# Performance work log

Hardware: AMD Instinct MI355X
Metric: run time of the kernel (lower is better)

## Reference

```python
import jax, jax.numpy as jnp
import numpy as np


def setup_inputs() -> dict:
    key = jax.random.key(0)
    ip = jax.random.normal(key, (8, 256, 128, 128), dtype=jnp.float32)
    return {"ip": ip}


def reference(ip):
    b, C, H, W = ip.shape
    two_c = 2 * C
    # precomputed complex shift grid: exp(-1j*2*pi*(C-0.5)*v/(2C)), v = 0..2C-1
    v = jnp.arange(two_c, dtype=jnp.float32)
    angle = -2.0 * jnp.pi * (C - 0.5) * v / two_c
    shift = (jnp.cos(angle) + 1j * jnp.sin(angle)).astype(jnp.complex64)  # [2C]

    viDct = ip * two_c                                   # [b, C, H, W]
    flip_neg = -viDct[:, 1:][:, ::-1]                    # [b, C-1, H, W]
    zeros = jnp.zeros((b, 1, H, W), dtype=ip.dtype)
    rev = jnp.concatenate([viDct, zeros, flip_neg], axis=1)  # [b, 2C, H, W]
    rev = rev.astype(jnp.complex64) * shift[None, :, None, None]
    vxx = jnp.fft.ifft(rev, axis=1)                      # norm='backward' (default)
    out = vxx[:, :C][:, ::-1].real                       # first C, flipped, real part
    return out.astype(ip.dtype)
```

## Files before the change

kernel.cpp:

```cpp
#include <hip/hip_runtime.h>
#include <hip/hip_bf16.h>
#include <math.h>

#define NB   8
#define NC   256
#define NHW  (128 * 128)

#define BM 128
#define BN 128
#define BK 32
#define LSTR 80

typedef __attribute__((ext_vector_type(4))) float f32x4;
typedef __attribute__((ext_vector_type(8))) short bf16x8;

__device__ __forceinline__ unsigned short f2bf(float f) {
    unsigned u = __builtin_bit_cast(unsigned, f);
    u += 0x7fffu + ((u >> 16) & 1u);
    return (unsigned short)(u >> 16);
}

__global__ void coef_kernel(unsigned short* __restrict__ coef) {
    int idx = blockIdx.x * 256 + threadIdx.x;
    int c = idx >> 8;
    int k = idx & 255;
    int t = (k * (2 * c + 1)) & 1023;
    float v = (k == 0) ? 1.0f : 2.0f * cosf((float)t * (float)(M_PI / 512.0));
    coef[idx] = f2bf(v);
}

__global__ __launch_bounds__(256, 2)
void dct_gemm(const float* __restrict__ X, const unsigned short* __restrict__ Mcoef,
              float* __restrict__ Out) {
    __shared__ unsigned char lds[2 * BM * LSTR];
    unsigned char* Alds = lds;
    unsigned char* Xlds = lds + BM * LSTR;

    const int tid  = threadIdx.x;
    const int lane = tid & 63;
    const int wave = tid >> 6;
    const int wm   = wave >> 1;
    const int wn   = wave & 1;
    const int m16  = lane & 15;
    const int quad = lane >> 4;

    const int p0 = blockIdx.x * BN;
    const int c0 = blockIdx.y * BM;
    const int bbase = blockIdx.z * (NC * NHW);

    const float* Xb = X + bbase;
    float* Ob = Out + bbase;

    const int sr = tid & 127;
    const int sh = tid >> 7;

    f32x4 acc[4][4];
#pragma unroll
    for (int i = 0; i < 4; i++)
#pragma unroll
        for (int j = 0; j < 4; j++) acc[i][j] = (f32x4){0.f, 0.f, 0.f, 0.f};

    for (int k0 = 0; k0 < NC; k0 += BK) {
        __syncthreads();

        {
            const unsigned short* src = Mcoef + (c0 + sr) * NC + k0 + sh * 16;
            int4 a0 = *(const int4*)(src);
            int4 a1 = *(const int4*)(src + 8);
            unsigned char* dst = Alds + sr * LSTR + sh * 32;
            *(int4*)(dst)      = a0;
            *(int4*)(dst + 16) = a1;
        }

        {
            const float* src = Xb + (k0 + sh * 16) * NHW + p0 + sr;
            float v[16];
#pragma unroll
            for (int j = 0; j < 16; j++) v[j] = src[j * NHW];
            unsigned pk[8];
#pragma unroll
            for (int j = 0; j < 8; j++) {
                unsigned lo = __builtin_bit_cast(unsigned, v[2 * j]);
                lo += 0x7fffu + ((lo >> 16) & 1u);
                unsigned hi = __builtin_bit_cast(unsigned, v[2 * j + 1]);
                hi += 0x7fffu + ((hi >> 16) & 1u);
                pk[j] = (lo >> 16) | (hi & 0xffff0000u);
            }
            unsigned char* dst = Xlds + sr * LSTR + sh * 32;
            *(int4*)(dst)      = (int4){(int)pk[0], (int)pk[1], (int)pk[2], (int)pk[3]};
            *(int4*)(dst + 16) = (int4){(int)pk[4], (int)pk[5], (int)pk[6], (int)pk[7]};
        }

        __syncthreads();

        bf16x8 afrag[4], bfrag[4];
#pragma unroll
        for (int mt = 0; mt < 4; mt++) {
            int row = wm * 64 + mt * 16 + m16;
            afrag[mt] = *(const bf16x8*)(Alds + row * LSTR + quad * 16);
        }
#pragma unroll
        for (int nt = 0; nt < 4; nt++) {
            int row = wn * 64 + nt * 16 + m16;
            bfrag[nt] = *(const bf16x8*)(Xlds + row * LSTR + quad * 16);
        }
#pragma unroll
        for (int mt = 0; mt < 4; mt++)
#pragma unroll
            for (int nt = 0; nt < 4; nt++)
                acc[mt][nt] = __builtin_amdgcn_mfma_f32_16x16x32_bf16(
                    afrag[mt], bfrag[nt], acc[mt][nt], 0, 0, 0);
    }

#pragma unroll
    for (int mt = 0; mt < 4; mt++) {
#pragma unroll
        for (int nt = 0; nt < 4; nt++) {
            int cc = c0 + wm * 64 + mt * 16 + quad * 4;
            int pp = p0 + wn * 64 + nt * 16 + m16;
            float* o = Ob + cc * NHW + pp;
#pragma unroll
            for (int r = 0; r < 4; r++)
                o[r * NHW] = acc[mt][nt][r];
        }
    }
}

extern "C" void kernel_launch(void* const* d_in, const int* in_sizes, int n_in,
                              void* d_out, int out_size, void* d_ws, size_t ws_size,
                              hipStream_t stream) {
    const float* ip = (const float*)d_in[0];
    float* out = (float*)d_out;
    unsigned short* coef = (unsigned short*)d_ws;

    coef_kernel<<<dim3(256), dim3(256), 0, stream>>>(coef);

    dim3 grid(NHW / BN, NC / BM, NB);
    dct_gemm<<<grid, dim3(256), 0, stream>>>(ip, coef, out);
}
```

Measured before the change: 248.3 us.

## Cover all channels per block, load coefficients to registers, double-buffer X

Each block now computes all 256 output channels for a 64-pixel tile, so the input is read from global memory once rather than once per channel block. The coefficient matrix fragments are loaded directly from global (cache-resident) into registers instead of staged through LDS. Input staging uses register prefetch and a double-buffered LDS tile with one barrier per k-step. This trades more per-block work and global coefficient reads for halved input traffic and fewer barriers.

```diff
diff --git a/kernel.cpp b/kernel.cpp
--- a/kernel.cpp
+++ b/kernel.cpp
@@ -6,18 +6,22 @@
 #define NC   256
 #define NHW  (128 * 128)
 
-#define BM 128
-#define BN 128
-#define BK 32
+#define BN   64
+#define BK   32
 #define LSTR 80
 
 typedef __attribute__((ext_vector_type(4))) float f32x4;
 typedef __attribute__((ext_vector_type(8))) short bf16x8;
 
-__device__ __forceinline__ unsigned short f2bf(float f) {
+__device__ __forceinline__ unsigned f2bf_hi(float f) {
     unsigned u = __builtin_bit_cast(unsigned, f);
     u += 0x7fffu + ((u >> 16) & 1u);
-    return (unsigned short)(u >> 16);
+    return u & 0xffff0000u;
+}
+__device__ __forceinline__ unsigned f2bf_lo(float f) {
+    unsigned u = __builtin_bit_cast(unsigned, f);
+    u += 0x7fffu + ((u >> 16) & 1u);
+    return u >> 16;
 }
 
 __global__ void coef_kernel(unsigned short* __restrict__ coef) {
@@ -26,15 +30,13 @@
     int k = idx & 255;
     int t = (k * (2 * c + 1)) & 1023;
     float v = (k == 0) ? 1.0f : 2.0f * cosf((float)t * (float)(M_PI / 512.0));
-    coef[idx] = f2bf(v);
+    coef[idx] = (unsigned short)f2bf_lo(v);
 }
 
-__global__ __launch_bounds__(256, 2)
+__global__ __launch_bounds__(512, 4)
 void dct_gemm(const float* __restrict__ X, const unsigned short* __restrict__ Mcoef,
               float* __restrict__ Out) {
-    __shared__ unsigned char lds[2 * BM * LSTR];
-    unsigned char* Alds = lds;
-    unsigned char* Xlds = lds + BM * LSTR;
+    __shared__ unsigned char Xlds[2 * BN * LSTR];
 
     const int tid  = threadIdx.x;
     const int lane = tid & 63;
@@ -45,79 +47,74 @@
     const int quad = lane >> 4;
 
     const int p0 = blockIdx.x * BN;
-    const int c0 = blockIdx.y * BM;
-    const int bbase = blockIdx.z * (NC * NHW);
+    const float* Xb = X + (size_t)blockIdx.y * (NC * NHW);
+    float* Ob = Out + (size_t)blockIdx.y * (NC * NHW);
 
-    const float* Xb = X + bbase;
-    float* Ob = Out + bbase;
+    const int sr = tid & 63;
+    const int sh = tid >> 6;
 
-    const int sr = tid & 127;
-    const int sh = tid >> 7;
-
-    f32x4 acc[4][4];
+    f32x4 acc[4][2];
 #pragma unroll
     for (int i = 0; i < 4; i++)
 #pragma unroll
-        for (int j = 0; j < 4; j++) acc[i][j] = (f32x4){0.f, 0.f, 0.f, 0.f};
+        for (int j = 0; j < 2; j++) acc[i][j] = (f32x4){0.f, 0.f, 0.f, 0.f};
 
-    for (int k0 = 0; k0 < NC; k0 += BK) {
+    const unsigned short* Abase = Mcoef + (wm * 64 + m16) * NC + quad * 8;
+    const float* Xsrc0 = Xb + p0 + sr;
+
+    float xv[4];
+#pragma unroll
+    for (int j = 0; j < 4; j++) xv[j] = Xsrc0[(sh * 4 + j) * NHW];
+    bf16x8 afr[4];
+#pragma unroll
+    for (int mt = 0; mt < 4; mt++)
+        afr[mt] = *(const bf16x8*)(Abase + mt * 16 * NC);
+
+    for (int it = 0; it < NC / BK; ++it) {
+        const int buf = (it & 1) * (BN * LSTR);
+
+        {
+            unsigned pk0 = f2bf_lo(xv[0]) | f2bf_hi(xv[1]);
+            unsigned pk1 = f2bf_lo(xv[2]) | f2bf_hi(xv[3]);
+            *(int2*)(Xlds + buf + sr * LSTR + sh * 8) = (int2){(int)pk0, (int)pk1};
+        }
         __syncthreads();
 
-        {
-            const unsigned short* src = Mcoef + (c0 + sr) * NC + k0 + sh * 16;
-            int4 a0 = *(const int4*)(src);
-            int4 a1 = *(const int4*)(src + 8);
-            unsigned char* dst = Alds + sr * LSTR + sh * 32;
-            *(int4*)(dst)      = a0;
-            *(int4*)(dst + 16) = a1;
+        const int nk0 = ((it + 1) & (NC / BK - 1)) * BK;
+        float xn[4];
+#pragma unroll
+        for (int j = 0; j < 4; j++) xn[j] = Xsrc0[(nk0 + sh * 4 + j) * NHW];
+        bf16x8 an[4];
+#pragma unroll
+        for (int mt = 0; mt < 4; mt++)
+            an[mt] = *(const bf16x8*)(Abase + mt * 16 * NC + nk0);
+
+        bf16x8 bfr[2];
+#pragma unroll
+        for (int nt = 0; nt < 2; nt++) {
+            int row = wn * 32 + nt * 16 + m16;
+            bfr[nt] = *(const bf16x8*)(Xlds + buf + row * LSTR + quad * 16);
         }
 
-        {
-            const float* src = Xb + (k0 + sh * 16) * NHW + p0 + sr;
-            float v[16];
-#pragma unroll
-            for (int j = 0; j < 16; j++) v[j] = src[j * NHW];
-            unsigned pk[8];
-#pragma unroll
-            for (int j = 0; j < 8; j++) {
-                unsigned lo = __builtin_bit_cast(unsigned, v[2 * j]);
-                lo += 0x7fffu + ((lo >> 16) & 1u);
-                unsigned hi = __builtin_bit_cast(unsigned, v[2 * j + 1]);
-                hi += 0x7fffu + ((hi >> 16) & 1u);
-                pk[j] = (lo >> 16) | (hi & 0xffff0000u);
-            }
-            unsigned char* dst = Xlds + sr * LSTR + sh * 32;
-            *(int4*)(dst)      = (int4){(int)pk[0], (int)pk[1], (int)pk[2], (int)pk[3]};
-            *(int4*)(dst + 16) = (int4){(int)pk[4], (int)pk[5], (int)pk[6], (int)pk[7]};
-        }
-
-        __syncthreads();
-
-        bf16x8 afrag[4], bfrag[4];
-#pragma unroll
-        for (int mt = 0; mt < 4; mt++) {
-            int row = wm * 64 + mt * 16 + m16;
-            afrag[mt] = *(const bf16x8*)(Alds + row * LSTR + quad * 16);
-        }
-#pragma unroll
-        for (int nt = 0; nt < 4; nt++) {
-            int row = wn * 64 + nt * 16 + m16;
-            bfrag[nt] = *(const bf16x8*)(Xlds + row * LSTR + quad * 16);
-        }
 #pragma unroll
         for (int mt = 0; mt < 4; mt++)
 #pragma unroll
-            for (int nt = 0; nt < 4; nt++)
+            for (int nt = 0; nt < 2; nt++)
                 acc[mt][nt] = __builtin_amdgcn_mfma_f32_16x16x32_bf16(
-                    afrag[mt], bfrag[nt], acc[mt][nt], 0, 0, 0);
+                    afr[mt], bfr[nt], acc[mt][nt], 0, 0, 0);
+
+#pragma unroll
+        for (int j = 0; j < 4; j++) xv[j] = xn[j];
+#pragma unroll
+        for (int mt = 0; mt < 4; mt++) afr[mt] = an[mt];
     }
 
 #pragma unroll
     for (int mt = 0; mt < 4; mt++) {
 #pragma unroll
-        for (int nt = 0; nt < 4; nt++) {
-            int cc = c0 + wm * 64 + mt * 16 + quad * 4;
-            int pp = p0 + wn * 64 + nt * 16 + m16;
+        for (int nt = 0; nt < 2; nt++) {
+            int cc = wm * 64 + mt * 16 + quad * 4;
+            int pp = p0 + wn * 32 + nt * 16 + m16;
             float* o = Ob + cc * NHW + pp;
 #pragma unroll
             for (int r = 0; r < 4; r++)
@@ -135,6 +132,6 @@
 
     coef_kernel<<<dim3(256), dim3(256), 0, stream>>>(coef);
 
-    dim3 grid(NHW / BN, NC / BM, NB);
-    dct_gemm<<<grid, dim3(256), 0, stream>>>(ip, coef, out);
+    dim3 grid(NHW / BN, NB);
+    dct_gemm<<<grid, dim3(512), 0, stream>>>(ip, coef, out);
 }
```

Result: slower. 260.0 us (+4.7%).
